# Performance work log

Hardware: AMD Instinct MI355X
Metric: run time of the kernel (lower is better)

The kernel has to match this reference:

```python
import jax, jax.numpy as jnp
import numpy as np

NEG = -9e15

def _gat_layer(x, adj, W, a_src, a_dst):
    # x: [B,N,Fin], W: [Fin,Fout], a_src/a_dst: [Fout], adj: [N,N]
    h = jnp.einsum('bnf,fo->bno', x, W)                    # [B,N,Fout]
    e_src = jnp.einsum('bno,o->bn', h, a_src)              # [B,N]
    e_dst = jnp.einsum('bno,o->bn', h, a_dst)              # [B,N]
    e = jax.nn.leaky_relu(e_src[:, :, None] + e_dst[:, None, :], 0.2)  # [B,N,N]
    att = jax.nn.softmax(jnp.where(adj > 0, e, NEG), axis=-1)
    return jnp.einsum('bij,bjo->bio', att, h)              # [B,N,Fout]

def setup_inputs() -> dict:
    key = jax.random.key(0)
    ks = jax.random.split(key, 12)
    B, N, Fin = 8, 2048, 128
    H = [128, 128, 64]
    C = 128
    s = lambda *d: 1.0 / np.sqrt(d[0])
    inp = {
        'x':   jax.random.normal(ks[0], (B, N, Fin), jnp.float32),
        'adj': jax.random.normal(ks[1], (N, N), jnp.float32),
        'W1':  jax.random.normal(ks[2], (Fin, H[0]), jnp.float32) * s(Fin),
        'a1s': jax.random.normal(ks[3], (H[0],), jnp.float32) * s(H[0]),
        'a1d': jax.random.normal(ks[4], (H[0],), jnp.float32) * s(H[0]),
        'W2':  jax.random.normal(ks[5], (H[0], H[1]), jnp.float32) * s(H[0]),
        'a2s': jax.random.normal(ks[6], (H[1],), jnp.float32) * s(H[1]),
        'a2d': jax.random.normal(ks[7], (H[1],), jnp.float32) * s(H[1]),
        'W3':  jax.random.normal(ks[8], (H[1], H[2]), jnp.float32) * s(H[1]),
        'a3s': jax.random.normal(ks[9], (H[2],), jnp.float32) * s(H[2]),
        'a3d': jax.random.normal(ks[10], (H[2],), jnp.float32) * s(H[2]),
        'Wlin': jax.random.normal(ks[11], (H[2] * N, C), jnp.float32) * s(H[2] * N),
        'blin': jnp.zeros((C,), jnp.float32),
    }
    return inp

def reference(x, adj, W1, a1s, a1d, W2, a2s, a2d, W3, a3s, a3d, Wlin, blin):
    out = jax.nn.relu(_gat_layer(x, adj, W1, a1s, a1d))
    out = jax.nn.relu(_gat_layer(out, adj, W2, a2s, a2d))
    out = jax.nn.relu(_gat_layer(out, adj, W3, a3s, a3d))
    B = out.shape[0]
    out = out.reshape(B, -1)              # flatten [B, N*H3]
    return out @ Wlin + blin              # [B, num_classes]
```

## Files before the change

### kernel.cpp

```cpp
#include <hip/hip_runtime.h>
#include <stdint.h>


typedef unsigned short u16;
typedef __bf16 bf16x8 __attribute__((ext_vector_type(8)));
typedef float f32x4 __attribute__((ext_vector_type(4)));
typedef u16 u16x8 __attribute__((ext_vector_type(8)));
typedef u16 u16x4 __attribute__((ext_vector_type(4)));

#define LOG2E 1.44269504088896340736f

__device__ __forceinline__ float b2f(u16 u) {
    union { unsigned int i; float f; } v; v.i = ((unsigned int)u) << 16; return v.f;
}
__device__ __forceinline__ u16 f2b(float f) {
    union { float f; unsigned int i; } v; v.f = f;
    unsigned int i = v.i;
    return (u16)((i + 0x7fffu + ((i >> 16) & 1u)) >> 16);
}
__device__ __forceinline__ float fast_exp2(float x) {
#if __has_builtin(__builtin_amdgcn_exp2f)
    return __builtin_amdgcn_exp2f(x);
#else
    return exp2f(x);
#endif
}

union ABfrag { bf16x8 v; u16x8 u; };

__global__ void __launch_bounds__(256) k_mask(const float* __restrict__ adj,
                                              uint32_t* __restrict__ adjm) {
    const int w = threadIdx.x >> 6, lane = threadIdx.x & 63;
    const int row = blockIdx.x * 4 + w;
    const float* ar = adj + (size_t)row * 2048;
    uint32_t* mr = adjm + (size_t)row * 64;
    for (int j0 = 0; j0 < 2048; j0 += 64) {
        unsigned long long m = __ballot(ar[j0 + lane] > 0.f);
        if (lane == 0) {
            mr[(j0 >> 5)] = (uint32_t)m;
            mr[(j0 >> 5) + 1] = (uint32_t)(m >> 32);
        }
    }
}

__global__ void k_prep(const float* __restrict__ W1, const float* __restrict__ W2,
                       const float* __restrict__ W3,
                       const float* __restrict__ a1s, const float* __restrict__ a1d,
                       const float* __restrict__ a2s, const float* __restrict__ a2d,
                       const float* __restrict__ a3s, const float* __restrict__ a3d,
                       u16* __restrict__ Wt1, u16* __restrict__ Wt2, u16* __restrict__ Wt3,
                       float* __restrict__ u1s, float* __restrict__ u1d,
                       float* __restrict__ u2s, float* __restrict__ u2d,
                       float* __restrict__ u3s, float* __restrict__ u3d) {
    if (blockIdx.x == 160) {
        int f = threadIdx.x;
        if (f < 128) {
            float s1 = 0.f, d1 = 0.f, s2 = 0.f, d2 = 0.f, s3 = 0.f, d3 = 0.f;
            for (int o = 0; o < 128; ++o) { float w = W1[f * 128 + o]; s1 += w * a1s[o]; d1 += w * a1d[o]; }
            for (int o = 0; o < 128; ++o) { float w = W2[f * 128 + o]; s2 += w * a2s[o]; d2 += w * a2d[o]; }
            for (int o = 0; o <  64; ++o) { float w = W3[f *  64 + o]; s3 += w * a3s[o]; d3 += w * a3d[o]; }
            u1s[f] = s1 * LOG2E; u1d[f] = d1 * LOG2E;
            u2s[f] = s2 * LOG2E; u2d[f] = d2 * LOG2E;
            u3s[f] = s3 * LOG2E; u3d[f] = d3 * LOG2E;
        }
        return;
    }
    int idx = blockIdx.x * 256 + threadIdx.x;
    if (idx < 16384) {
        int f = idx >> 7, o = idx & 127;
        Wt1[o * 128 + f] = f2b(W1[idx]);
    } else if (idx < 32768) {
        int j = idx - 16384; int f = j >> 7, o = j & 127;
        Wt2[o * 128 + f] = f2b(W2[j]);
    } else if (idx < 40960) {
        int j = idx - 32768; int f = j >> 6, o = j & 63;
        Wt3[o * 128 + f] = f2b(W3[j]);
    }
}

template <int F, bool XF32>
__global__ void __launch_bounds__(256) k_h(const void* __restrict__ xv,
                                           const u16* __restrict__ Wt,
                                           const float* __restrict__ us,
                                           const float* __restrict__ ud,
                                           u16* __restrict__ h_t,
                                           float* __restrict__ esf,
                                           float* __restrict__ edf) {
    constexpr int NTB = F / 32;
    constexpr int TNP = 72;
    __shared__ __align__(16) u16 hl[(F / 2) * TNP];

    const int b = blockIdx.x;
    const int nb2 = blockIdx.y;
    const int nblk = nb2 >> 1, ohalf = nb2 & 1;
    const int tid = threadIdx.x;
    const int w = tid >> 6, lane = tid & 63;
    const int quad = lane >> 4, l15 = lane & 15;
    const int n0w = nblk * 64 + w * 16;
    const int i_a = n0w + l15;

    ABfrag afr[4];
    float ps = 0.f, pd = 0.f;
    if (XF32) {
        const float* xr = (const float*)xv + ((size_t)(b * 2048 + i_a)) * 128;
#pragma unroll
        for (int kk = 0; kk < 4; ++kk) {
            const int o8 = kk * 32 + quad * 8;
            float4 x0 = *reinterpret_cast<const float4*>(xr + o8);
            float4 x1 = *reinterpret_cast<const float4*>(xr + o8 + 4);
            float4 s0 = *reinterpret_cast<const float4*>(us + o8);
            float4 s1 = *reinterpret_cast<const float4*>(us + o8 + 4);
            float4 d0 = *reinterpret_cast<const float4*>(ud + o8);
            float4 d1 = *reinterpret_cast<const float4*>(ud + o8 + 4);
            ps += x0.x * s0.x + x0.y * s0.y + x0.z * s0.z + x0.w * s0.w
                + x1.x * s1.x + x1.y * s1.y + x1.z * s1.z + x1.w * s1.w;
            pd += x0.x * d0.x + x0.y * d0.y + x0.z * d0.z + x0.w * d0.w
                + x1.x * d1.x + x1.y * d1.y + x1.z * d1.z + x1.w * d1.w;
            afr[kk].u[0] = f2b(x0.x); afr[kk].u[1] = f2b(x0.y);
            afr[kk].u[2] = f2b(x0.z); afr[kk].u[3] = f2b(x0.w);
            afr[kk].u[4] = f2b(x1.x); afr[kk].u[5] = f2b(x1.y);
            afr[kk].u[6] = f2b(x1.z); afr[kk].u[7] = f2b(x1.w);
        }
    } else {
        const u16* xr = (const u16*)xv + ((size_t)(b * 2048 + i_a)) * 128;
#pragma unroll
        for (int kk = 0; kk < 4; ++kk) {
            const int o8 = kk * 32 + quad * 8;
            u16x8 xa = *reinterpret_cast<const u16x8*>(xr + o8);
            afr[kk].u = xa;
            float4 s0 = *reinterpret_cast<const float4*>(us + o8);
            float4 s1 = *reinterpret_cast<const float4*>(us + o8 + 4);
            float4 d0 = *reinterpret_cast<const float4*>(ud + o8);
            float4 d1 = *reinterpret_cast<const float4*>(ud + o8 + 4);
            float xf[8];
#pragma unroll
            for (int j = 0; j < 8; ++j) xf[j] = b2f(xa[j]);
            ps += xf[0] * s0.x + xf[1] * s0.y + xf[2] * s0.z + xf[3] * s0.w
                + xf[4] * s1.x + xf[5] * s1.y + xf[6] * s1.z + xf[7] * s1.w;
            pd += xf[0] * d0.x + xf[1] * d0.y + xf[2] * d0.z + xf[3] * d0.w
                + xf[4] * d1.x + xf[5] * d1.y + xf[6] * d1.z + xf[7] * d1.w;
        }
    }
    if (ohalf == 0) {
        ps += __shfl_xor(ps, 16, 64); ps += __shfl_xor(ps, 32, 64);
        pd += __shfl_xor(pd, 16, 64); pd += __shfl_xor(pd, 32, 64);
        if (quad == 0) {
            const size_t idx = (size_t)(b * 2048 + i_a) * 2;
            float2 sv; sv.x = fast_exp2(ps); sv.y = fast_exp2(0.2f * ps);
            float2 dv; dv.x = fast_exp2(pd); dv.y = fast_exp2(0.2f * pd);
            *reinterpret_cast<float2*>(esf + idx) = sv;
            *reinterpret_cast<float2*>(edf + idx) = dv;
        }
    }

    f32x4 acc[NTB];
#pragma unroll
    for (int nt = 0; nt < NTB; ++nt) acc[nt] = (f32x4){0.f, 0.f, 0.f, 0.f};
#pragma unroll
    for (int kk = 0; kk < 4; ++kk) {
#pragma unroll
        for (int nt = 0; nt < NTB; ++nt) {
            bf16x8 bfv = *reinterpret_cast<const bf16x8*>(
                Wt + (ohalf * (F / 2) + nt * 16 + l15) * 128 + kk * 32 + quad * 8);
            acc[nt] = __builtin_amdgcn_mfma_f32_16x16x32_bf16(afr[kk].v, bfv, acc[nt], 0, 0, 0);
        }
    }

#pragma unroll
    for (int nt = 0; nt < NTB; ++nt)
#pragma unroll
        for (int r = 0; r < 4; ++r)
            hl[(nt * 16 + l15) * TNP + w * 16 + quad * 4 + r] = f2b(acc[nt][r]);
    __syncthreads();
    if (tid < F) {
        int o_loc = tid >> 1, half32 = tid & 1;
        const u16* src = hl + o_loc * TNP + half32 * 32;
        u16* dst = h_t + ((size_t)(b * F + ohalf * (F / 2) + o_loc)) * 2048
                   + nblk * 64 + half32 * 32;
#pragma unroll
        for (int c = 0; c < 4; ++c)
            *reinterpret_cast<u16x8*>(dst + c * 8) =
                *reinterpret_cast<const u16x8*>(src + c * 8);
    }
}

template <int F, bool OUT_F32>
__global__ void __launch_bounds__(256, 2) k_attn(const float* __restrict__ esf,
                                                 const float* __restrict__ edf,
                                                 const uint32_t* __restrict__ adjm,
                                                 const u16* __restrict__ h_t,
                                                 void* __restrict__ outp) {
    constexpr int NT = F / 16;
    constexpr int LP_BYTES = 4096 * 4 + 2048 * 4;
    constexpr int CB_BYTES = 4 * 32 * F * 4 + 4 * 32 * 4;
    constexpr int LDS_BYTES = (LP_BYTES > CB_BYTES) ? LP_BYTES : CB_BYTES;
    __shared__ __align__(16) char Sraw[LDS_BYTES];
    float* eL = (float*)Sraw;
    uint32_t* mL = (uint32_t*)(Sraw + 4096 * 4);
    float* part = (float*)Sraw;
    float* denp = (float*)(Sraw + 4 * 32 * F * 4);

    const int b = blockIdx.x;
    const int i32blk = blockIdx.y;
    const int i0 = i32blk * 32;
    const int tid = threadIdx.x;
    const int w = tid >> 6;
    const int lane = tid & 63;
    const int quad = lane >> 4, l15 = lane & 15;
    const int r0 = l15, r1 = l15 + 16;

    const float2 e0p = *reinterpret_cast<const float2*>(esf + ((size_t)(b * 2048 + i0 + r0)) * 2);
    const float2 e1p = *reinterpret_cast<const float2*>(esf + ((size_t)(b * 2048 + i0 + r1)) * 2);
    const float Es0 = e0p.x, Fs0 = e0p.y, Es1 = e1p.x, Fs1 = e1p.y;
    const u16* hb = h_t + (size_t)b * F * 2048;

    ABfrag onesf;
#pragma unroll
    for (int j = 0; j < 8; ++j) onesf.u[j] = 0x3F80;

    f32x4 acc0[NT], acc1[NT];
#pragma unroll
    for (int nt = 0; nt < NT; ++nt) {
        acc0[nt] = (f32x4){0.f, 0.f, 0.f, 0.f};
        acc1[nt] = (f32x4){0.f, 0.f, 0.f, 0.f};
    }
    f32x4 d0 = (f32x4){0.f, 0.f, 0.f, 0.f};
    f32x4 d1 = (f32x4){0.f, 0.f, 0.f, 0.f};

    {
        const float4* esrc = (const float4*)(edf + (size_t)b * 4096);
        float4* edst = (float4*)eL;
#pragma unroll
        for (int t = 0; t < 4; ++t) edst[tid + t * 256] = esrc[tid + t * 256];
        const uint2* msrc = (const uint2*)(adjm + (size_t)i0 * 64);
#pragma unroll
        for (int t = 0; t < 4; ++t) {
            int idx = tid + t * 256;
            int r = idx >> 5, k2 = idx & 31;
            uint2 v = msrc[idx];
            mL[r * 64 + ((2 * k2) ^ r)] = v.x;
            mL[r * 64 + ((2 * k2 + 1) ^ r)] = v.y;
        }
    }
    __syncthreads();

    const int jbase = w * 16;
    auto loadB = [&](int t, ABfrag* bt) {
        const size_t coff = (size_t)((jbase + t) * 32 + quad * 8);
#pragma unroll
        for (int nt = 0; nt < NT; ++nt)
            bt[nt].u = *reinterpret_cast<const u16x8*>(
                hb + (size_t)(nt * 16 + l15) * 2048 + coff);
    };

    ABfrag bt[NT], bn[NT];
    loadB(0, bt);

    for (int t = 0; t < 16; ++t) {
        if (t < 15) loadB(t + 1, bn);
        const int jt = jbase + t;
        const int j0 = jt * 32;

        f32x4 ec[4];
        {
            const float* ep = eL + (size_t)(j0 + quad * 8) * 2;
#pragma unroll
            for (int q = 0; q < 4; ++q) ec[q] = *reinterpret_cast<const f32x4*>(ep + q * 4);
        }
        const uint32_t m0 = mL[r0 * 64 + (jt ^ r0)];
        const uint32_t m1 = mL[r1 * 64 + (jt ^ r1)];

        ABfrag af0, af1;
#pragma unroll
        for (int px = 0; px < 4; ++px) {
            const f32x4 q = ec[px];
            const int bsh = quad * 8 + px * 2;
            float wa0 = fmaxf(Es0 * q.x, Fs0 * q.y);
            float wb0 = fmaxf(Es0 * q.z, Fs0 * q.w);
            float wa1 = fmaxf(Es1 * q.x, Fs1 * q.y);
            float wb1 = fmaxf(Es1 * q.z, Fs1 * q.w);
            const uint32_t sa0 = 0u - ((m0 >> bsh) & 1u);
            const uint32_t sb0 = 0u - ((m0 >> (bsh + 1)) & 1u);
            const uint32_t sa1 = 0u - ((m1 >> bsh) & 1u);
            const uint32_t sb1 = 0u - ((m1 >> (bsh + 1)) & 1u);
            wa0 = __uint_as_float(__float_as_uint(wa0) & sa0);
            wb0 = __uint_as_float(__float_as_uint(wb0) & sb0);
            wa1 = __uint_as_float(__float_as_uint(wa1) & sa1);
            wb1 = __uint_as_float(__float_as_uint(wb1) & sb1);
            af0.v[px * 2]     = (__bf16)wa0;
            af0.v[px * 2 + 1] = (__bf16)wb0;
            af1.v[px * 2]     = (__bf16)wa1;
            af1.v[px * 2 + 1] = (__bf16)wb1;
        }

#pragma unroll
        for (int nt = 0; nt < NT; ++nt) {
            acc0[nt] = __builtin_amdgcn_mfma_f32_16x16x32_bf16(af0.v, bt[nt].v, acc0[nt], 0, 0, 0);
            acc1[nt] = __builtin_amdgcn_mfma_f32_16x16x32_bf16(af1.v, bt[nt].v, acc1[nt], 0, 0, 0);
        }
        d0 = __builtin_amdgcn_mfma_f32_16x16x32_bf16(af0.v, onesf.v, d0, 0, 0, 0);
        d1 = __builtin_amdgcn_mfma_f32_16x16x32_bf16(af1.v, onesf.v, d1, 0, 0, 0);

        if (t < 15) {
#pragma unroll
            for (int nt = 0; nt < NT; ++nt) bt[nt] = bn[nt];
        }
    }

    __syncthreads();
    {
        float* pw = part + (size_t)w * 32 * F;
#pragma unroll
        for (int nt = 0; nt < NT; ++nt)
#pragma unroll
            for (int r = 0; r < 4; ++r) {
                pw[(quad * 4 + r) * F + nt * 16 + l15] = acc0[nt][r];
                pw[(16 + quad * 4 + r) * F + nt * 16 + l15] = acc1[nt][r];
            }
#pragma unroll
        for (int r = 0; r < 4; ++r) {
            denp[w * 32 + quad * 4 + r] = d0[r];
            denp[w * 32 + 16 + quad * 4 + r] = d1[r];
        }
    }
    __syncthreads();
    {
        constexpr int C4 = F / 4;
        for (int idx = tid; idx < 32 * C4; idx += 256) {
            const int row = idx / C4, c4 = idx % C4;
            f32x4 s = *reinterpret_cast<const f32x4*>(&part[row * F + c4 * 4]);
#pragma unroll
            for (int ww = 1; ww < 4; ++ww)
                s += *reinterpret_cast<const f32x4*>(&part[(ww * 32 + row) * F + c4 * 4]);
            const float den = denp[row] + denp[32 + row] + denp[64 + row] + denp[96 + row];
            const float dinv = 1.0f / fmaxf(den, 1e-30f);
            if (OUT_F32) {
                float4 o;
                o.x = fmaxf(s[0] * dinv, 0.f); o.y = fmaxf(s[1] * dinv, 0.f);
                o.z = fmaxf(s[2] * dinv, 0.f); o.w = fmaxf(s[3] * dinv, 0.f);
                *reinterpret_cast<float4*>((float*)outp +
                    ((size_t)(b * 2048 + i0 + row)) * F + c4 * 4) = o;
            } else {
                u16x4 o;
                o[0] = f2b(fmaxf(s[0] * dinv, 0.f)); o[1] = f2b(fmaxf(s[1] * dinv, 0.f));
                o[2] = f2b(fmaxf(s[2] * dinv, 0.f)); o[3] = f2b(fmaxf(s[3] * dinv, 0.f));
                *reinterpret_cast<u16x4*>((u16*)outp +
                    ((size_t)(b * 2048 + i0 + row)) * F + c4 * 4) = o;
            }
        }
    }
}

__global__ void __launch_bounds__(256) k_lin(const float* __restrict__ o3,
                                             const float* __restrict__ Wlin,
                                             float* __restrict__ pbuf) {
    __shared__ float xc[8][256];
    __shared__ float red[8][8][128];
    const int tid = threadIdx.x;
    const int k0 = blockIdx.x * 256;
    for (int idx = tid; idx < 2048; idx += 256) {
        int bb = idx >> 8, kk = idx & 255;
        xc[bb][kk] = o3[(size_t)bb * 131072 + k0 + kk];
    }
    __syncthreads();
    const int o4 = tid & 31;
    const int kb = tid >> 5;
    f32x4 acc[8];
#pragma unroll
    for (int bb = 0; bb < 8; ++bb) acc[bb] = (f32x4){0.f, 0.f, 0.f, 0.f};
    const float* wp = Wlin + (size_t)(k0 + kb * 32) * 128 + o4 * 4;
#pragma unroll 4
    for (int k = 0; k < 32; ++k) {
        f32x4 wv = *reinterpret_cast<const f32x4*>(wp + (size_t)k * 128);
#pragma unroll
        for (int bb = 0; bb < 8; ++bb) acc[bb] += wv * xc[bb][kb * 32 + k];
    }
#pragma unroll
    for (int bb = 0; bb < 8; ++bb)
        *reinterpret_cast<f32x4*>(&red[kb][bb][o4 * 4]) = acc[bb];
    __syncthreads();
    const int f = tid * 4;
    const int bb = f >> 7, o = f & 127;
    f32x4 s = (f32x4){0.f, 0.f, 0.f, 0.f};
#pragma unroll
    for (int k2 = 0; k2 < 8; ++k2) s += *reinterpret_cast<const f32x4*>(&red[k2][bb][o]);
    *reinterpret_cast<f32x4*>(&pbuf[(size_t)blockIdx.x * 1024 + f]) = s;
}

__global__ void __launch_bounds__(256) k_bias(const float* __restrict__ pbuf,
                                              const float* __restrict__ blin,
                                              float* __restrict__ out) {
    __shared__ float red[256];
    const int tid = threadIdx.x;
    const int p16 = tid >> 4;
    const int fo = tid & 15;
    const int f0 = blockIdx.x * 16;
    float s = 0.f;
#pragma unroll 4
    for (int p = p16; p < 512; p += 16)
        s += pbuf[(size_t)p * 1024 + f0 + fo];
    red[tid] = s;
    __syncthreads();
    if (tid < 16) {
        float t = 0.f;
#pragma unroll
        for (int k = 0; k < 16; ++k) t += red[k * 16 + tid];
        out[f0 + tid] = t + blin[(f0 + tid) & 127];
    }
}

extern "C" void kernel_launch(void* const* d_in, const int* in_sizes, int n_in,
                              void* d_out, int out_size, void* d_ws, size_t ws_size,
                              hipStream_t stream) {
    (void)in_sizes; (void)n_in; (void)out_size;
    const float* x    = (const float*)d_in[0];
    const float* adj  = (const float*)d_in[1];
    const float* W1   = (const float*)d_in[2];
    const float* a1s  = (const float*)d_in[3];
    const float* a1d  = (const float*)d_in[4];
    const float* W2   = (const float*)d_in[5];
    const float* a2s  = (const float*)d_in[6];
    const float* a2d  = (const float*)d_in[7];
    const float* W3   = (const float*)d_in[8];
    const float* a3s  = (const float*)d_in[9];
    const float* a3d  = (const float*)d_in[10];
    const float* Wlin = (const float*)d_in[11];
    const float* blin = (const float*)d_in[12];

    char* ws = (char*)d_ws;
    u16*   h_t = (u16*)ws;
    size_t off = (size_t)4 << 20;
    float* esf = (float*)(ws + off); off += 131072;
    float* edf = (float*)(ws + off); off += 131072;
    u16*   Wt1 = (u16*)(ws + off);   off += 32768;
    u16*   Wt2 = (u16*)(ws + off);   off += 32768;
    u16*   Wt3 = (u16*)(ws + off);   off += 16384;
    float* u1s = (float*)(ws + off); off += 512;
    float* u1d = (float*)(ws + off); off += 512;
    float* u2s = (float*)(ws + off); off += 512;
    float* u2d = (float*)(ws + off); off += 512;
    float* u3s = (float*)(ws + off); off += 512;
    float* u3d = (float*)(ws + off); off += 512;
    uint32_t* adjm = (uint32_t*)(ws + off); off += 524288;
    float* pbuf = (float*)(ws + off); off += (size_t)512 * 1024 * 4;
    u16* actA;
    if (ws_size >= off + ((size_t)4 << 20)) {
        actA = (u16*)(ws + off);
    } else {
        actA = (u16*)d_in[0];
    }
    float* o3 = (float*)actA;

    dim3 ga(8, 64);
    dim3 gh(8, 64);
    k_mask<<<512, 256, 0, stream>>>(adj, adjm);
    k_prep<<<161, 256, 0, stream>>>(W1, W2, W3, a1s, a1d, a2s, a2d, a3s, a3d,
                                    Wt1, Wt2, Wt3, u1s, u1d, u2s, u2d, u3s, u3d);

    k_h<128, true ><<<gh, 256, 0, stream>>>((const void*)x, Wt1, u1s, u1d, h_t, esf, edf);
    k_attn<128, false><<<ga, 256, 0, stream>>>(esf, edf, adjm, h_t, (void*)actA);

    k_h<128, false><<<gh, 256, 0, stream>>>((const void*)actA, Wt2, u2s, u2d, h_t, esf, edf);
    k_attn<128, false><<<ga, 256, 0, stream>>>(esf, edf, adjm, h_t, (void*)actA);

    k_h<64, false><<<gh, 256, 0, stream>>>((const void*)actA, Wt3, u3s, u3d, h_t, esf, edf);
    k_attn<64, true ><<<ga, 256, 0, stream>>>(esf, edf, adjm, h_t, (void*)o3);

    k_lin<<<512, 256, 0, stream>>>(o3, Wlin, pbuf);
    k_bias<<<64, 256, 0, stream>>>(pbuf, blin, (float*)d_out);
}
```

Measured before the change: 270.1 us.

## Split attention output features across grid z, change e_dst layout, double-buffer B loads

```diff
diff --git a/kernel.cpp b/kernel.cpp
--- a/kernel.cpp
+++ b/kernel.cpp
@@ -5,6 +5,7 @@
 typedef unsigned short u16;
 typedef __bf16 bf16x8 __attribute__((ext_vector_type(8)));
 typedef float f32x4 __attribute__((ext_vector_type(4)));
+typedef float f32x2 __attribute__((ext_vector_type(2)));
 typedef u16 u16x8 __attribute__((ext_vector_type(8)));
 typedef u16 u16x4 __attribute__((ext_vector_type(4)));
 
@@ -145,11 +146,10 @@
         ps += __shfl_xor(ps, 16, 64); ps += __shfl_xor(ps, 32, 64);
         pd += __shfl_xor(pd, 16, 64); pd += __shfl_xor(pd, 32, 64);
         if (quad == 0) {
-            const size_t idx = (size_t)(b * 2048 + i_a) * 2;
             float2 sv; sv.x = fast_exp2(ps); sv.y = fast_exp2(0.2f * ps);
-            float2 dv; dv.x = fast_exp2(pd); dv.y = fast_exp2(0.2f * pd);
-            *reinterpret_cast<float2*>(esf + idx) = sv;
-            *reinterpret_cast<float2*>(edf + idx) = dv;
+            *reinterpret_cast<float2*>(esf + (size_t)(b * 2048 + i_a) * 2) = sv;
+            edf[(size_t)b * 4096 + i_a]        = fast_exp2(pd);
+            edf[(size_t)b * 4096 + 2048 + i_a] = fast_exp2(0.2f * pd);
         }
     }
 
@@ -185,24 +185,27 @@
 }
 
 template <int F, bool OUT_F32>
-__global__ void __launch_bounds__(256, 2) k_attn(const float* __restrict__ esf,
+__global__ void __launch_bounds__(256, 4) k_attn(const float* __restrict__ esf,
                                                  const float* __restrict__ edf,
                                                  const uint32_t* __restrict__ adjm,
                                                  const u16* __restrict__ h_t,
                                                  void* __restrict__ outp) {
-    constexpr int NT = F / 16;
-    constexpr int LP_BYTES = 4096 * 4 + 2048 * 4;
-    constexpr int CB_BYTES = 4 * 32 * F * 4 + 4 * 32 * 4;
+    constexpr int FH  = F / 2;
+    constexpr int NT2 = FH / 16;
+    constexpr int LP_BYTES = 8192 + 8192 + 8192;
+    constexpr int CB_BYTES = 4 * 32 * FH * 4 + 512;
     constexpr int LDS_BYTES = (LP_BYTES > CB_BYTES) ? LP_BYTES : CB_BYTES;
     __shared__ __align__(16) char Sraw[LDS_BYTES];
-    float* eL = (float*)Sraw;
-    uint32_t* mL = (uint32_t*)(Sraw + 4096 * 4);
+    float* EdL = (float*)Sraw;
+    float* FdL = (float*)(Sraw + 8192);
+    uint32_t* mL = (uint32_t*)(Sraw + 16384);
     float* part = (float*)Sraw;
-    float* denp = (float*)(Sraw + 4 * 32 * F * 4);
+    float* denp = (float*)(Sraw + 4 * 32 * FH * 4);
 
     const int b = blockIdx.x;
-    const int i32blk = blockIdx.y;
-    const int i0 = i32blk * 32;
+    const int i0 = blockIdx.y * 32;
+    const int ch = blockIdx.z;
+    const int c0 = ch * FH;
     const int tid = threadIdx.x;
     const int w = tid >> 6;
     const int lane = tid & 63;
@@ -218,20 +221,25 @@
 #pragma unroll
     for (int j = 0; j < 8; ++j) onesf.u[j] = 0x3F80;
 
-    f32x4 acc0[NT], acc1[NT];
-#pragma unroll
-    for (int nt = 0; nt < NT; ++nt) {
+    f32x4 acc0[NT2], acc1[NT2];
+#pragma unroll
+    for (int nt = 0; nt < NT2; ++nt) {
         acc0[nt] = (f32x4){0.f, 0.f, 0.f, 0.f};
         acc1[nt] = (f32x4){0.f, 0.f, 0.f, 0.f};
     }
-    f32x4 d0 = (f32x4){0.f, 0.f, 0.f, 0.f};
-    f32x4 d1 = (f32x4){0.f, 0.f, 0.f, 0.f};
+    f32x4 dn0 = (f32x4){0.f, 0.f, 0.f, 0.f};
+    f32x4 dn1 = (f32x4){0.f, 0.f, 0.f, 0.f};
 
     {
-        const float4* esrc = (const float4*)(edf + (size_t)b * 4096);
-        float4* edst = (float4*)eL;
-#pragma unroll
-        for (int t = 0; t < 4; ++t) edst[tid + t * 256] = esrc[tid + t * 256];
+        const float4* eds = (const float4*)(edf + (size_t)b * 4096);
+        const float4* fds = (const float4*)(edf + (size_t)b * 4096 + 2048);
+        float4* edd = (float4*)EdL;
+        float4* fdd = (float4*)FdL;
+#pragma unroll
+        for (int t = 0; t < 2; ++t) {
+            edd[tid + t * 256] = eds[tid + t * 256];
+            fdd[tid + t * 256] = fds[tid + t * 256];
+        }
         const uint2* msrc = (const uint2*)(adjm + (size_t)i0 * 64);
 #pragma unroll
         for (int t = 0; t < 4; ++t) {
@@ -248,90 +256,86 @@
     auto loadB = [&](int t, ABfrag* bt) {
         const size_t coff = (size_t)((jbase + t) * 32 + quad * 8);
 #pragma unroll
-        for (int nt = 0; nt < NT; ++nt)
+        for (int nt = 0; nt < NT2; ++nt)
             bt[nt].u = *reinterpret_cast<const u16x8*>(
-                hb + (size_t)(nt * 16 + l15) * 2048 + coff);
+                hb + (size_t)(c0 + nt * 16 + l15) * 2048 + coff);
     };
 
-    ABfrag bt[NT], bn[NT];
-    loadB(0, bt);
-
-    for (int t = 0; t < 16; ++t) {
-        if (t < 15) loadB(t + 1, bn);
+    auto computeTile = [&](int t, ABfrag* bt) {
         const int jt = jbase + t;
         const int j0 = jt * 32;
-
-        f32x4 ec[4];
-        {
-            const float* ep = eL + (size_t)(j0 + quad * 8) * 2;
-#pragma unroll
-            for (int q = 0; q < 4; ++q) ec[q] = *reinterpret_cast<const f32x4*>(ep + q * 4);
-        }
-        const uint32_t m0 = mL[r0 * 64 + (jt ^ r0)];
-        const uint32_t m1 = mL[r1 * 64 + (jt ^ r1)];
+        const uint32_t mm0 = mL[r0 * 64 + (jt ^ r0)] >> (quad * 8);
+        const uint32_t mm1 = mL[r1 * 64 + (jt ^ r1)] >> (quad * 8);
+        const f32x2* edp = (const f32x2*)(EdL + j0 + quad * 8);
+        const f32x2* fdp = (const f32x2*)(FdL + j0 + quad * 8);
 
         ABfrag af0, af1;
 #pragma unroll
-        for (int px = 0; px < 4; ++px) {
-            const f32x4 q = ec[px];
-            const int bsh = quad * 8 + px * 2;
-            float wa0 = fmaxf(Es0 * q.x, Fs0 * q.y);
-            float wb0 = fmaxf(Es0 * q.z, Fs0 * q.w);
-            float wa1 = fmaxf(Es1 * q.x, Fs1 * q.y);
-            float wb1 = fmaxf(Es1 * q.z, Fs1 * q.w);
-            const uint32_t sa0 = 0u - ((m0 >> bsh) & 1u);
-            const uint32_t sb0 = 0u - ((m0 >> (bsh + 1)) & 1u);
-            const uint32_t sa1 = 0u - ((m1 >> bsh) & 1u);
-            const uint32_t sb1 = 0u - ((m1 >> (bsh + 1)) & 1u);
-            wa0 = __uint_as_float(__float_as_uint(wa0) & sa0);
-            wb0 = __uint_as_float(__float_as_uint(wb0) & sb0);
-            wa1 = __uint_as_float(__float_as_uint(wa1) & sa1);
-            wb1 = __uint_as_float(__float_as_uint(wb1) & sb1);
-            af0.v[px * 2]     = (__bf16)wa0;
-            af0.v[px * 2 + 1] = (__bf16)wb0;
-            af1.v[px * 2]     = (__bf16)wa1;
-            af1.v[px * 2 + 1] = (__bf16)wb1;
-        }
-
-#pragma unroll
-        for (int nt = 0; nt < NT; ++nt) {
+        for (int p = 0; p < 4; ++p) {
+            const f32x2 ed = edp[p];
+            const f32x2 fd = fdp[p];
+            f32x2 a0 = ed * Es0, b0 = fd * Fs0;
+            f32x2 a1 = ed * Es1, b1 = fd * Fs1;
+            float w0x = fmaxf(a0.x, b0.x), w0y = fmaxf(a0.y, b0.y);
+            float w1x = fmaxf(a1.x, b1.x), w1y = fmaxf(a1.y, b1.y);
+            const int s0x = ((int)(mm0 << (31 - (p * 2)))) >> 31;
+            const int s0y = ((int)(mm0 << (31 - (p * 2 + 1)))) >> 31;
+            const int s1x = ((int)(mm1 << (31 - (p * 2)))) >> 31;
+            const int s1y = ((int)(mm1 << (31 - (p * 2 + 1)))) >> 31;
+            w0x = __uint_as_float(__float_as_uint(w0x) & (uint32_t)s0x);
+            w0y = __uint_as_float(__float_as_uint(w0y) & (uint32_t)s0y);
+            w1x = __uint_as_float(__float_as_uint(w1x) & (uint32_t)s1x);
+            w1y = __uint_as_float(__float_as_uint(w1y) & (uint32_t)s1y);
+            af0.v[p * 2]     = (__bf16)w0x;
+            af0.v[p * 2 + 1] = (__bf16)w0y;
+            af1.v[p * 2]     = (__bf16)w1x;
+            af1.v[p * 2 + 1] = (__bf16)w1y;
+        }
+        __builtin_amdgcn_s_setprio(1);
+#pragma unroll
+        for (int nt = 0; nt < NT2; ++nt) {
             acc0[nt] = __builtin_amdgcn_mfma_f32_16x16x32_bf16(af0.v, bt[nt].v, acc0[nt], 0, 0, 0);
             acc1[nt] = __builtin_amdgcn_mfma_f32_16x16x32_bf16(af1.v, bt[nt].v, acc1[nt], 0, 0, 0);
         }
-        d0 = __builtin_amdgcn_mfma_f32_16x16x32_bf16(af0.v, onesf.v, d0, 0, 0, 0);
-        d1 = __builtin_amdgcn_mfma_f32_16x16x32_bf16(af1.v, onesf.v, d1, 0, 0, 0);
-
-        if (t < 15) {
-#pragma unroll
-            for (int nt = 0; nt < NT; ++nt) bt[nt] = bn[nt];
-        }
+        dn0 = __builtin_amdgcn_mfma_f32_16x16x32_bf16(af0.v, onesf.v, dn0, 0, 0, 0);
+        dn1 = __builtin_amdgcn_mfma_f32_16x16x32_bf16(af1.v, onesf.v, dn1, 0, 0, 0);
+        __builtin_amdgcn_s_setprio(0);
+    };
+
+    ABfrag btA[NT2], btB[NT2];
+    loadB(0, btA);
+    for (int t = 0; t < 16; t += 2) {
+        loadB(t + 1, btB);
+        computeTile(t, btA);
+        if (t + 2 < 16) loadB(t + 2, btA);
+        computeTile(t + 1, btB);
     }
 
     __syncthreads();
     {
-        float* pw = part + (size_t)w * 32 * F;
-#pragma unroll
-        for (int nt = 0; nt < NT; ++nt)
+        float* pw = part + (size_t)w * 32 * FH;
+#pragma unroll
+        for (int nt = 0; nt < NT2; ++nt)
 #pragma unroll
             for (int r = 0; r < 4; ++r) {
-                pw[(quad * 4 + r) * F + nt * 16 + l15] = acc0[nt][r];
-                pw[(16 + quad * 4 + r) * F + nt * 16 + l15] = acc1[nt][r];
+                pw[(quad * 4 + r) * FH + nt * 16 + l15] = acc0[nt][r];
+                pw[(16 + quad * 4 + r) * FH + nt * 16 + l15] = acc1[nt][r];
             }
 #pragma unroll
         for (int r = 0; r < 4; ++r) {
-            denp[w * 32 + quad * 4 + r] = d0[r];
-            denp[w * 32 + 16 + quad * 4 + r] = d1[r];
+            denp[w * 32 + quad * 4 + r] = dn0[r];
+            denp[w * 32 + 16 + quad * 4 + r] = dn1[r];
         }
     }
     __syncthreads();
     {
-        constexpr int C4 = F / 4;
+        constexpr int C4 = FH / 4;
         for (int idx = tid; idx < 32 * C4; idx += 256) {
             const int row = idx / C4, c4 = idx % C4;
-            f32x4 s = *reinterpret_cast<const f32x4*>(&part[row * F + c4 * 4]);
+            f32x4 s = *reinterpret_cast<const f32x4*>(&part[row * FH + c4 * 4]);
 #pragma unroll
             for (int ww = 1; ww < 4; ++ww)
-                s += *reinterpret_cast<const f32x4*>(&part[(ww * 32 + row) * F + c4 * 4]);
+                s += *reinterpret_cast<const f32x4*>(&part[(ww * 32 + row) * FH + c4 * 4]);
             const float den = denp[row] + denp[32 + row] + denp[64 + row] + denp[96 + row];
             const float dinv = 1.0f / fmaxf(den, 1e-30f);
             if (OUT_F32) {
@@ -339,13 +343,13 @@
                 o.x = fmaxf(s[0] * dinv, 0.f); o.y = fmaxf(s[1] * dinv, 0.f);
                 o.z = fmaxf(s[2] * dinv, 0.f); o.w = fmaxf(s[3] * dinv, 0.f);
                 *reinterpret_cast<float4*>((float*)outp +
-                    ((size_t)(b * 2048 + i0 + row)) * F + c4 * 4) = o;
+                    ((size_t)(b * 2048 + i0 + row)) * F + c0 + c4 * 4) = o;
             } else {
                 u16x4 o;
                 o[0] = f2b(fmaxf(s[0] * dinv, 0.f)); o[1] = f2b(fmaxf(s[1] * dinv, 0.f));
                 o[2] = f2b(fmaxf(s[2] * dinv, 0.f)); o[3] = f2b(fmaxf(s[3] * dinv, 0.f));
                 *reinterpret_cast<u16x4*>((u16*)outp +
-                    ((size_t)(b * 2048 + i0 + row)) * F + c4 * 4) = o;
+                    ((size_t)(b * 2048 + i0 + row)) * F + c0 + c4 * 4) = o;
             }
         }
     }
@@ -451,7 +455,7 @@
     }
     float* o3 = (float*)actA;
 
-    dim3 ga(8, 64);
+    dim3 ga(8, 64, 2);
     dim3 gh(8, 64);
     k_mask<<<512, 256, 0, stream>>>(adj, adjm);
     k_prep<<<161, 256, 0, stream>>>(W1, W2, W3, a1s, a1d, a2s, a2d, a3s, a3d,
```

Result: slower. 276.6 us (+2.4%).
